# Kernel optimization log

Measured on AMD Instinct MI355X. Metric: run time of the kernel, lower is better.

Reference implementation:

```python
import jax, jax.numpy as jnp
import numpy as np

S, B, D = 2048, 2, 1024
NH, DH, DI = 16, 64, 4096


def setup_inputs() -> dict:
    key = jax.random.key(0)
    ks = jax.random.split(key, 12)
    init_qkv = 1.0 / np.sqrt(D)
    init_out = 1.0 / np.sqrt(NH * DH)
    stdm = 1.0 / np.sqrt(D)
    stdi = 1.0 / np.sqrt(DI)

    def u(k, shape, lo, hi):
        return jax.random.uniform(k, shape, jnp.float32, lo, hi)

    inp = {}
    inp["dec_inp"] = jax.random.normal(ks[0], (S, B, D), jnp.float32)
    # causal mask: True = masked (future key j > query i); shape [q, k, batch]
    causal = jnp.triu(jnp.ones((S, S), bool), k=1)
    inp["attn_mask"] = jnp.broadcast_to(causal[:, :, None], (S, S, B))
    inp["query_mean"] = u(ks[1], (NH * DH, D), -init_qkv, init_qkv)
    inp["key_mean"] = u(ks[2], (NH * DH, D), -init_qkv, init_qkv)
    inp["value_mean"] = u(ks[3], (NH * DH, D), -init_qkv, init_qkv)
    inp["query_std"] = u(ks[4], (NH * DH, D), 2 * np.log(init_qkv), np.log(init_qkv))
    inp["key_std"] = u(ks[5], (NH * DH, D), 2 * np.log(init_qkv), np.log(init_qkv))
    inp["value_std"] = u(ks[6], (NH * DH, D), 2 * np.log(init_qkv), np.log(init_qkv))
    inp["output_mean"] = u(ks[7], (D, NH * DH), -init_out, init_out)
    inp["output_std"] = u(ks[8], (D, NH * DH), 2 * np.log(init_out), np.log(init_out))
    inp["ln1_gamma"] = jnp.ones((D,), jnp.float32)
    inp["ln1_beta"] = jnp.zeros((D,), jnp.float32)
    inp["w1_mean"] = u(ks[9], (DI, D), -stdm, stdm)
    inp["w2_mean"] = u(ks[10], (D, DI), -stdi, stdi)
    inp["w1_std"] = u(ks[11], (DI, D), 2 * np.log(stdm), np.log(stdm))
    inp["w2_std"] = u(jax.random.fold_in(key, 99), (D, DI), 2 * np.log(stdi), np.log(stdi))
    inp["ln2_gamma"] = jnp.ones((D,), jnp.float32)
    inp["ln2_beta"] = jnp.zeros((D,), jnp.float32)
    return inp


def _layer_norm(x, g, b, eps=1e-5):
    mu = jnp.mean(x, -1, keepdims=True)
    var = jnp.mean((x - mu) ** 2, -1, keepdims=True)
    return g * (x - mu) * jax.lax.rsqrt(var + eps) + b


def _kl(theta_mean, theta_std):
    return jnp.mean(theta_mean ** 2 - 2.0 * theta_std + jnp.exp(2.0 * theta_std)) / 2.0


def reference(dec_inp, attn_mask, query_mean, key_mean, value_mean, query_std,
              key_std, value_std, output_mean, output_std, ln1_gamma, ln1_beta,
              w1_mean, w2_mean, w1_std, w2_std, ln2_gamma, ln2_beta):
    scale = 1.0 / (DH ** 0.5)
    # QKV projections (eval mode: no Bayesian weight sampling, diffs are 0)
    head_q = jnp.einsum('ibd,hd->ibh', dec_inp, query_mean).reshape(S, B, NH, DH)
    head_k = jnp.einsum('ibd,hd->ibh', dec_inp, key_mean).reshape(S, B, NH, DH)
    head_v = jnp.einsum('ibd,hd->ibh', dec_inp, value_mean).reshape(S, B, NH, DH)
    attn_score = jnp.einsum('ibnd,jbnd->ijbn', head_q, head_k) * scale
    attn_score = jnp.where(attn_mask[:, :, :, None], -jnp.inf, attn_score)
    attn_prob = jax.nn.softmax(attn_score, axis=1)  # softmax over key dim j
    attn_vec = jnp.einsum('ijbn,jbnd->ibnd', attn_prob, head_v).reshape(S, B, NH * DH)
    # NOTE: the original code (bug-faithfully) projects with value_mean, not output_mean
    attn_out = jnp.einsum('ibh,dh->ibd', attn_vec, value_mean)
    h = _layer_norm(dec_inp + attn_out, ln1_gamma, ln1_beta)
    attn_kl = _kl(
        jnp.concatenate([query_mean, key_mean, value_mean, output_mean.T], -1),
        jnp.concatenate([query_std, key_std, value_std, output_std.T], -1))
    # Bayesian positionwise FF (no activation in BayesPositionwiseFF)
    l1 = jnp.einsum('ibd,fd->ibf', h, w1_mean)
    l2 = jnp.einsum('ibf,df->ibd', l1, w2_mean)
    out = _layer_norm(h + l2, ln2_gamma, ln2_beta)
    ff_kl = _kl(jnp.concatenate([w1_mean, w2_mean.T], -1),
                jnp.concatenate([w1_std, w2_std.T], -1))
    return out, attn_kl + ff_kl
```

## Files before the change

### kernel.cpp

```cpp
#include <hip/hip_runtime.h>

#define S_LEN  2048
#define BATCH  2
#define DMODEL 1024
#define NHEADS 16
#define DHEAD  64
#define DFF    4096
#define MROWS  (S_LEN*BATCH)
#define QKVN   3072

typedef __attribute__((ext_vector_type(8))) short bf16x8;
typedef __attribute__((ext_vector_type(4))) float f32x4;
typedef __attribute__((ext_vector_type(4))) short s16x4;

#define NEG_BIG (-3.0e38f)
#define SCALE_LOG2 (0.125f * 1.4426950408889634f)

__device__ __forceinline__ short f2bf(float f){
  unsigned u = __float_as_uint(f);
  u += 0x7fffu + ((u >> 16) & 1u);
  return (short)(u >> 16);
}

__device__ __forceinline__ void gload16(const void* gptr, void* lptr){
  __builtin_amdgcn_global_load_lds(
      (const __attribute__((address_space(1))) unsigned int*)gptr,
      (__attribute__((address_space(3))) unsigned int*)lptr,
      16, 0, 0);
}

__global__ __launch_bounds__(256) void cast_kernel(const float* __restrict__ in,
                                                   short* __restrict__ out, int n){
  int i = (blockIdx.x * 256 + threadIdx.x) * 4;
  if (i >= n) return;
  f32x4 v = *(const f32x4*)(in + i);
  s16x4 o;
  o[0] = f2bf(v[0]); o[1] = f2bf(v[1]); o[2] = f2bf(v[2]); o[3] = f2bf(v[3]);
  *(s16x4*)(out + i) = o;
}

__global__ __launch_bounds__(256) void cast_kl_kernel(const float* __restrict__ mean,
                                                      const float* __restrict__ stdv,
                                                      short* __restrict__ outb,
                                                      int n, double* acc){
  __shared__ double red[4];
  double local = 0.0;
  const int stride = gridDim.x * 1024;
  for (int i = (blockIdx.x * 256 + threadIdx.x) * 4; i < n; i += stride){
    f32x4 m = *(const f32x4*)(mean + i);
    f32x4 sv = *(const f32x4*)(stdv + i);
    if (outb){
      s16x4 o;
      o[0] = f2bf(m[0]); o[1] = f2bf(m[1]); o[2] = f2bf(m[2]); o[3] = f2bf(m[3]);
      *(s16x4*)(outb + i) = o;
    }
    for (int e = 0; e < 4; e++)
      local += (double)(m[e] * m[e]) - 2.0 * (double)sv[e] + (double)expf(2.f * sv[e]);
  }
  for (int msk = 1; msk < 64; msk <<= 1) local += __shfl_xor(local, msk, 64);
  const int t = threadIdx.x;
  if ((t & 63) == 0) red[t >> 6] = local;
  __syncthreads();
  if (t == 0) atomicAdd(acc, red[0] + red[1] + red[2] + red[3]);
}

__global__ void kl_final(const double* acc, float* out){
  out[0] = (float)(acc[0] / 8388608.0 + acc[1] / 16777216.0);
}

template<int BN>
__global__ __launch_bounds__(512) void gemm_bt(const short* __restrict__ A,
                                               const short* __restrict__ Bt,
                                               float* __restrict__ Cf,
                                               short* __restrict__ Cb,
                                               int M, int N, int K, int nbx){
  __shared__ short As[4][128][32];
  __shared__ short Bs[4][BN][32];
  constexpr int NB = BN / 32;
  constexpr int BSTRIDE = BN * 64;
  const int t = threadIdx.x;
  const int lane = t & 63, w = t >> 6;
  const int q8 = (int)gridDim.x >> 3;
  const int sid = ((int)blockIdx.x & 7) * q8 + ((int)blockIdx.x >> 3);
  const int bx = sid % nbx, by = sid / nbx;
  const int m0 = by * 128, n0 = bx * BN;
  const int wm = (w & 3) * 32, wn = (w >> 2) * (BN / 2);
  const int lr = lane & 15, lg = lane >> 4;
  const bool doB = (BN == 128) || (t < 256);
  const bool twoLoads = (BN == 128) || (w < 4);

  f32x4 acc[2][NB] = {};

  const short* Ap = A  + (size_t)(m0 + (t >> 2)) * K + (t & 3) * 8;
  const short* Bp = Bt + (size_t)(n0 + ((t & (BN * 4 - 1)) >> 2)) * K + (t & 3) * 8;
  char* ldsA0 = (char*)As + w * 1024;
  char* ldsB0 = (char*)Bs + (w & (NB * 2 - 1)) * 1024;

  const int nk = K / 32;
  for (int p = 0; p < 3; p++){
    gload16(Ap + p * 32, ldsA0 + p * 8192);
    if (doB) gload16(Bp + p * 32, ldsB0 + p * BSTRIDE);
  }

  for (int kt = 0; kt < nk; kt++){
    const int rem = nk - 1 - kt;
    if (twoLoads){
      if (rem >= 2)      asm volatile("s_waitcnt vmcnt(4)" ::: "memory");
      else if (rem == 1) asm volatile("s_waitcnt vmcnt(2)" ::: "memory");
      else               asm volatile("s_waitcnt vmcnt(0)" ::: "memory");
    } else {
      if (rem >= 2)      asm volatile("s_waitcnt vmcnt(2)" ::: "memory");
      else if (rem == 1) asm volatile("s_waitcnt vmcnt(1)" ::: "memory");
      else               asm volatile("s_waitcnt vmcnt(0)" ::: "memory");
    }
    __builtin_amdgcn_s_barrier();
    asm volatile("" ::: "memory");

    const int nxt = kt + 3;
    if (nxt < nk){
      gload16(Ap + nxt * 32, ldsA0 + (nxt & 3) * 8192);
      if (doB) gload16(Bp + nxt * 32, ldsB0 + (nxt & 3) * BSTRIDE);
    }

    const int cur = kt & 3;
    bf16x8 a0 = *(const bf16x8*)&As[cur][wm      + lr][lg * 8];
    bf16x8 a1 = *(const bf16x8*)&As[cur][wm + 16 + lr][lg * 8];
    bf16x8 bfr[NB];
    for (int ni = 0; ni < NB; ni++)
      bfr[ni] = *(const bf16x8*)&Bs[cur][wn + ni * 16 + lr][lg * 8];
    __builtin_amdgcn_s_setprio(1);
    for (int ni = 0; ni < NB; ni++){
      acc[0][ni] = __builtin_amdgcn_mfma_f32_16x16x32_bf16(a0, bfr[ni], acc[0][ni], 0, 0, 0);
      acc[1][ni] = __builtin_amdgcn_mfma_f32_16x16x32_bf16(a1, bfr[ni], acc[1][ni], 0, 0, 0);
    }
    __builtin_amdgcn_s_setprio(0);
  }

  for (int mi = 0; mi < 2; mi++){
    for (int ni = 0; ni < NB; ni++){
      int row = m0 + wm + mi * 16 + lg * 4;
      int col = n0 + wn + ni * 16 + lr;
      for (int r = 0; r < 4; r++){
        float v = acc[mi][ni][r];
        if (Cf) Cf[(size_t)(row + r) * N + col] = v;
        if (Cb) Cb[(size_t)(row + r) * N + col] = f2bf(v);
      }
    }
  }
}

__global__ __launch_bounds__(256) void attn_kernel(const short* __restrict__ QKV,
                                                   short* __restrict__ AV){
  __shared__ short Ks[64][64];
  __shared__ short Vst[64][64];
  __shared__ short Pt[4][16][64];
  const int t = threadIdx.x, lane = t & 63, w = t >> 6;
  const int hb = blockIdx.y;
  const int b = hb >> 4, n = hb & 15;
  const int lr = lane & 15, lg = lane >> 4;

  const int qt = 31 - (int)blockIdx.x;
  const int q0w = qt * 64 + w * 16;

  bf16x8 aq[2];
  {
    const short* qp = QKV + ((size_t)(q0w + lr) * BATCH + b) * QKVN + n * DHEAD + lg * 8;
    aq[0] = *(const bf16x8*)(qp);
    aq[1] = *(const bf16x8*)(qp + 32);
  }

  f32x4 acc[4] = {};
  float m_run = NEG_BIG, l_run = 0.f;

  for (int jt = 0; jt <= qt; jt++){
    const int j0 = jt * 64;
    __syncthreads();
    {
      int j = t >> 2, u0 = (t & 3) * 2;
      const short* kp = QKV + ((size_t)(j0 + j) * BATCH + b) * QKVN + DMODEL + n * DHEAD + u0 * 8;
      *(bf16x8*)&Ks[j][(u0 ^ (j & 7)) * 8]       = *(const bf16x8*)(kp);
      *(bf16x8*)&Ks[j][((u0 + 1) ^ (j & 7)) * 8] = *(const bf16x8*)(kp + 8);
      int jv = t & 63, dq = (t >> 6) * 16;
      const short* vp = QKV + ((size_t)(j0 + jv) * BATCH + b) * QKVN + 2 * DMODEL + n * DHEAD + dq;
      bf16x8 v0 = *(const bf16x8*)(vp);
      bf16x8 v1 = *(const bf16x8*)(vp + 8);
      int uj = jv >> 3, jl = jv & 7;
      for (int e = 0; e < 8; e++){
        int sc = (((uj ^ e) << 3) | jl);
        Vst[dq + e][sc]     = v0[e];
        Vst[dq + 8 + e][sc] = v1[e];
      }
    }
    __syncthreads();

    f32x4 s[4];
    __builtin_amdgcn_s_setprio(1);
    for (int nf = 0; nf < 4; nf++){
      f32x4 z = {};
      for (int kk = 0; kk < 2; kk++){
        bf16x8 bk = *(const bf16x8*)&Ks[nf * 16 + lr][((kk * 4 + lg) ^ (lr & 7)) * 8];
        z = __builtin_amdgcn_mfma_f32_16x16x32_bf16(bk, aq[kk], z, 0, 0, 0);
      }
      s[nf] = z;
    }
    __builtin_amdgcn_s_setprio(0);

    if (jt == qt){
      int qg = q0w + lr;
      for (int nf = 0; nf < 4; nf++)
        for (int r = 0; r < 4; r++)
          if (j0 + nf * 16 + lg * 4 + r > qg) s[nf][r] = NEG_BIG;
    }

    float mx = NEG_BIG;
    for (int nf = 0; nf < 4; nf++){
      float a0 = fmaxf(s[nf][0], s[nf][1]);
      float a1 = fmaxf(s[nf][2], s[nf][3]);
      mx = fmaxf(mx, fmaxf(a0, a1));
    }
    mx = fmaxf(mx, __shfl_xor(mx, 16, 64));
    mx = fmaxf(mx, __shfl_xor(mx, 32, 64));
    float mxs = mx * SCALE_LOG2;

    if (__any(mxs > m_run + 8.f)){
      float mn = fmaxf(m_run, mxs);
      float corr = __builtin_exp2f(m_run - mn);
      m_run = mn;
      l_run *= corr;
      float cb[4];
      for (int r = 0; r < 4; r++) cb[r] = __shfl(corr, lg * 4 + r, 64);
      for (int df = 0; df < 4; df++)
        for (int r = 0; r < 4; r++) acc[df][r] *= cb[r];
    }

    float rs = 0.f;
    for (int nf = 0; nf < 4; nf++)
      for (int r = 0; r < 4; r++){
        float p = __builtin_exp2f(fmaf(s[nf][r], SCALE_LOG2, -m_run));
        s[nf][r] = p;
        rs += p;
      }
    rs += __shfl_xor(rs, 16, 64);
    rs += __shfl_xor(rs, 32, 64);
    l_run += rs;

    char* prow = (char*)&Pt[w][lr][0];
    for (int nf = 0; nf < 4; nf++){
      unsigned u0 = __float_as_uint(s[nf][0]);
      unsigned u1 = __float_as_uint(s[nf][1]);
      unsigned u2 = __float_as_uint(s[nf][2]);
      unsigned u3 = __float_as_uint(s[nf][3]);
      uint2 val;
      val.x = (u0 >> 16) | (u1 & 0xffff0000u);
      val.y = (u2 >> 16) | (u3 & 0xffff0000u);
      int off = ((((nf * 2) + (lg >> 1)) ^ (lr & 7)) << 4) + ((lg & 1) << 3);
      *(uint2*)(prow + off) = val;
    }

    __builtin_amdgcn_s_setprio(1);
    for (int kk = 0; kk < 2; kk++){
      bf16x8 pa = *(const bf16x8*)(prow + ((((kk * 4) + lg) ^ (lr & 7)) << 4));
      for (int df = 0; df < 4; df++){
        bf16x8 bv = *(const bf16x8*)&Vst[df * 16 + lr][((kk * 4 + lg) ^ (lr & 7)) * 8];
        acc[df] = __builtin_amdgcn_mfma_f32_16x16x32_bf16(pa, bv, acc[df], 0, 0, 0);
      }
    }
    __builtin_amdgcn_s_setprio(0);
  }

  float lb[4];
  for (int r = 0; r < 4; r++) lb[r] = __shfl(l_run, lg * 4 + r, 64);
  for (int df = 0; df < 4; df++){
    for (int r = 0; r < 4; r++){
      int i_glob = q0w + lg * 4 + r;
      AV[((size_t)i_glob * BATCH + b) * DMODEL + n * DHEAD + df * 16 + lr] =
          f2bf(acc[df][r] / lb[r]);
    }
  }
}

__global__ __launch_bounds__(256) void ln_kernel(const float* __restrict__ xa,
                                                 const float* __restrict__ xb,
                                                 const float* __restrict__ gamma,
                                                 const float* __restrict__ beta,
                                                 float* __restrict__ outF,
                                                 short* __restrict__ outB){
  __shared__ float red[4];
  const int row = blockIdx.x, t = threadIdx.x;
  const size_t base = (size_t)row * DMODEL + t * 4;
  f32x4 a  = *(const f32x4*)(xa + base);
  f32x4 bb = *(const f32x4*)(xb + base);
  f32x4 x;
  for (int e = 0; e < 4; e++) x[e] = a[e] + bb[e];
  float sum = x[0] + x[1] + x[2] + x[3];
  for (int m = 1; m < 64; m <<= 1) sum += __shfl_xor(sum, m, 64);
  if ((t & 63) == 0) red[t >> 6] = sum;
  __syncthreads();
  float mu = (red[0] + red[1] + red[2] + red[3]) * (1.f / DMODEL);
  float sq = 0.f;
  for (int e = 0; e < 4; e++){ float d = x[e] - mu; sq += d * d; }
  for (int m = 1; m < 64; m <<= 1) sq += __shfl_xor(sq, m, 64);
  __syncthreads();
  if ((t & 63) == 0) red[t >> 6] = sq;
  __syncthreads();
  float var = (red[0] + red[1] + red[2] + red[3]) * (1.f / DMODEL);
  float rstd = rsqrtf(var + 1e-5f);
  f32x4 g  = *(const f32x4*)(gamma + t * 4);
  f32x4 be = *(const f32x4*)(beta + t * 4);
  for (int e = 0; e < 4; e++){
    float y = g[e] * (x[e] - mu) * rstd + be[e];
    if (outF) outF[base + e] = y;
    if (outB) outB[base + e] = f2bf(y);
  }
}

extern "C" void kernel_launch(void* const* d_in, const int* in_sizes, int n_in,
                              void* d_out, int out_size, void* d_ws, size_t ws_size,
                              hipStream_t stream){
  (void)in_sizes; (void)n_in; (void)out_size; (void)ws_size;
  const float* dec = (const float*)d_in[0];
  const float* qm  = (const float*)d_in[2];
  const float* km  = (const float*)d_in[3];
  const float* vm  = (const float*)d_in[4];
  const float* qs  = (const float*)d_in[5];
  const float* ks  = (const float*)d_in[6];
  const float* vs  = (const float*)d_in[7];
  const float* om  = (const float*)d_in[8];
  const float* os_ = (const float*)d_in[9];
  const float* g1  = (const float*)d_in[10];
  const float* b1  = (const float*)d_in[11];
  const float* w1m = (const float*)d_in[12];
  const float* w2m = (const float*)d_in[13];
  const float* w1s = (const float*)d_in[14];
  const float* w2s = (const float*)d_in[15];
  const float* g2  = (const float*)d_in[16];
  const float* b2  = (const float*)d_in[17];
  float* out = (float*)d_out;

  char* ws = (char*)d_ws;
  size_t off = 0;
  auto alloc = [&](size_t bytes) -> char* {
    char* p = ws + off;
    off += (bytes + 255) & ~(size_t)255;
    return p;
  };
  short* Xb   = (short*)alloc((size_t)MROWS * DMODEL * 2);
  short* Wqkv = (short*)alloc((size_t)QKVN * DMODEL * 2);
  short* W1   = (short*)alloc((size_t)DFF * DMODEL * 2);
  short* W2   = (short*)alloc((size_t)DMODEL * DFF * 2);
  short* Wv   = Wqkv + (size_t)2 * DMODEL * DMODEL;
  short* QKVb = (short*)alloc((size_t)MROWS * QKVN * 2);
  short* AVb  = (short*)alloc((size_t)MROWS * DMODEL * 2);
  float* tmpF = (float*)alloc((size_t)MROWS * DMODEL * 4);
  float* hF   = (float*)alloc((size_t)MROWS * DMODEL * 4);
  double* acc = (double*)alloc(256);
  short* L1 = QKVb;

  hipMemsetAsync(acc, 0, 16, stream);

  cast_kernel<<<MROWS * DMODEL / 1024, 256, 0, stream>>>(dec, Xb, MROWS * DMODEL);
  cast_kl_kernel<<<1024, 256, 0, stream>>>(qm, qs, Wqkv, DMODEL * DMODEL, acc);
  cast_kl_kernel<<<1024, 256, 0, stream>>>(km, ks, Wqkv + (size_t)DMODEL * DMODEL, DMODEL * DMODEL, acc);
  cast_kl_kernel<<<1024, 256, 0, stream>>>(vm, vs, Wqkv + (size_t)2 * DMODEL * DMODEL, DMODEL * DMODEL, acc);
  cast_kl_kernel<<<1024, 256, 0, stream>>>(om, os_, nullptr, DMODEL * DMODEL, acc);
  cast_kl_kernel<<<1024, 256, 0, stream>>>(w1m, w1s, W1, DFF * DMODEL, acc + 1);
  cast_kl_kernel<<<1024, 256, 0, stream>>>(w2m, w2s, W2, DMODEL * DFF, acc + 1);

  gemm_bt<128><<<(QKVN / 128) * (MROWS / 128), 512, 0, stream>>>(Xb, Wqkv, nullptr, QKVb, MROWS, QKVN, DMODEL, QKVN / 128);

  attn_kernel<<<dim3(32, BATCH * NHEADS), 256, 0, stream>>>(QKVb, AVb);

  gemm_bt<64><<<(DMODEL / 64) * (MROWS / 128), 512, 0, stream>>>(AVb, Wv, tmpF, nullptr, MROWS, DMODEL, DMODEL, DMODEL / 64);

  ln_kernel<<<MROWS, 256, 0, stream>>>(dec, tmpF, g1, b1, hF, Xb);

  gemm_bt<128><<<(DFF / 128) * (MROWS / 128), 512, 0, stream>>>(Xb, W1, nullptr, L1, MROWS, DFF, DMODEL, DFF / 128);
  gemm_bt<64><<<(DMODEL / 64) * (MROWS / 128), 512, 0, stream>>>(L1, W2, tmpF, nullptr, MROWS, DMODEL, DFF, DMODEL / 64);

  ln_kernel<<<MROWS, 256, 0, stream>>>(hF, tmpF, g2, b2, out, nullptr);

  kl_final<<<1, 1, 0, stream>>>(acc, out + (size_t)MROWS * DMODEL);
}
```

Baseline: 565.9 us.

## Pair causal query tiles per attention block and use triple-buffered GEMM pipeline

The attention kernel now launches half as many blocks, and each block processes query tile i and tile 31-i so every block does the same amount of causal work, removing tail imbalance. Separately, the GEMM shared-memory pipeline drops from four stages to three, with a prefetch distance of two and simpler waitcnt logic. This reduces LDS use, which may allow more blocks per CU, but gives less load-latency hiding. The attention change also halves the grid to 512 blocks, which may leave the GPU less occupied.

```diff
diff --git a/kernel.cpp b/kernel.cpp
--- a/kernel.cpp
+++ b/kernel.cpp
@@ -74,8 +74,8 @@
                                                float* __restrict__ Cf,
                                                short* __restrict__ Cb,
                                                int M, int N, int K, int nbx){
-  __shared__ short As[4][128][32];
-  __shared__ short Bs[4][BN][32];
+  __shared__ short As[3][128][32];
+  __shared__ short Bs[3][BN][32];
   constexpr int NB = BN / 32;
   constexpr int BSTRIDE = BN * 64;
   const int t = threadIdx.x;
@@ -87,7 +87,6 @@
   const int wm = (w & 3) * 32, wn = (w >> 2) * (BN / 2);
   const int lr = lane & 15, lg = lane >> 4;
   const bool doB = (BN == 128) || (t < 256);
-  const bool twoLoads = (BN == 128) || (w < 4);
 
   f32x4 acc[2][NB] = {};
 
@@ -97,43 +96,40 @@
   char* ldsB0 = (char*)Bs + (w & (NB * 2 - 1)) * 1024;
 
   const int nk = K / 32;
-  for (int p = 0; p < 3; p++){
+  for (int p = 0; p < 2; p++){
     gload16(Ap + p * 32, ldsA0 + p * 8192);
     if (doB) gload16(Bp + p * 32, ldsB0 + p * BSTRIDE);
   }
 
+  int bufcur = 0;
   for (int kt = 0; kt < nk; kt++){
-    const int rem = nk - 1 - kt;
-    if (twoLoads){
-      if (rem >= 2)      asm volatile("s_waitcnt vmcnt(4)" ::: "memory");
-      else if (rem == 1) asm volatile("s_waitcnt vmcnt(2)" ::: "memory");
-      else               asm volatile("s_waitcnt vmcnt(0)" ::: "memory");
+    if (kt + 1 < nk){
+      if (doB) asm volatile("s_waitcnt vmcnt(2)" ::: "memory");
+      else     asm volatile("s_waitcnt vmcnt(1)" ::: "memory");
     } else {
-      if (rem >= 2)      asm volatile("s_waitcnt vmcnt(2)" ::: "memory");
-      else if (rem == 1) asm volatile("s_waitcnt vmcnt(1)" ::: "memory");
-      else               asm volatile("s_waitcnt vmcnt(0)" ::: "memory");
+      asm volatile("s_waitcnt vmcnt(0)" ::: "memory");
     }
     __builtin_amdgcn_s_barrier();
     asm volatile("" ::: "memory");
 
-    const int nxt = kt + 3;
-    if (nxt < nk){
-      gload16(Ap + nxt * 32, ldsA0 + (nxt & 3) * 8192);
-      if (doB) gload16(Bp + nxt * 32, ldsB0 + (nxt & 3) * BSTRIDE);
-    }
-
-    const int cur = kt & 3;
-    bf16x8 a0 = *(const bf16x8*)&As[cur][wm      + lr][lg * 8];
-    bf16x8 a1 = *(const bf16x8*)&As[cur][wm + 16 + lr][lg * 8];
+    if (kt + 2 < nk){
+      int bnx = bufcur >= 1 ? bufcur - 1 : bufcur + 2;
+      gload16(Ap + (kt + 2) * 32, ldsA0 + bnx * 8192);
+      if (doB) gload16(Bp + (kt + 2) * 32, ldsB0 + bnx * BSTRIDE);
+    }
+
+    bf16x8 a0 = *(const bf16x8*)&As[bufcur][wm      + lr][lg * 8];
+    bf16x8 a1 = *(const bf16x8*)&As[bufcur][wm + 16 + lr][lg * 8];
     bf16x8 bfr[NB];
     for (int ni = 0; ni < NB; ni++)
-      bfr[ni] = *(const bf16x8*)&Bs[cur][wn + ni * 16 + lr][lg * 8];
+      bfr[ni] = *(const bf16x8*)&Bs[bufcur][wn + ni * 16 + lr][lg * 8];
     __builtin_amdgcn_s_setprio(1);
     for (int ni = 0; ni < NB; ni++){
       acc[0][ni] = __builtin_amdgcn_mfma_f32_16x16x32_bf16(a0, bfr[ni], acc[0][ni], 0, 0, 0);
       acc[1][ni] = __builtin_amdgcn_mfma_f32_16x16x32_bf16(a1, bfr[ni], acc[1][ni], 0, 0, 0);
     }
     __builtin_amdgcn_s_setprio(0);
+    bufcur = bufcur < 2 ? bufcur + 1 : 0;
   }
 
   for (int mi = 0; mi < 2; mi++){
@@ -159,123 +155,126 @@
   const int b = hb >> 4, n = hb & 15;
   const int lr = lane & 15, lg = lane >> 4;
 
-  const int qt = 31 - (int)blockIdx.x;
-  const int q0w = qt * 64 + w * 16;
-
-  bf16x8 aq[2];
-  {
-    const short* qp = QKV + ((size_t)(q0w + lr) * BATCH + b) * QKVN + n * DHEAD + lg * 8;
-    aq[0] = *(const bf16x8*)(qp);
-    aq[1] = *(const bf16x8*)(qp + 32);
-  }
-
-  f32x4 acc[4] = {};
-  float m_run = NEG_BIG, l_run = 0.f;
-
-  for (int jt = 0; jt <= qt; jt++){
-    const int j0 = jt * 64;
+  for (int half = 0; half < 2; half++){
+    const int qt = half ? (31 - (int)blockIdx.x) : (int)blockIdx.x;
+    const int q0w = qt * 64 + w * 16;
+
+    bf16x8 aq[2];
+    {
+      const short* qp = QKV + ((size_t)(q0w + lr) * BATCH + b) * QKVN + n * DHEAD + lg * 8;
+      aq[0] = *(const bf16x8*)(qp);
+      aq[1] = *(const bf16x8*)(qp + 32);
+    }
+
+    f32x4 acc[4] = {};
+    float m_run = NEG_BIG, l_run = 0.f;
+
+    for (int jt = 0; jt <= qt; jt++){
+      const int j0 = jt * 64;
+      __syncthreads();
+      {
+        int j = t >> 2, u0 = (t & 3) * 2;
+        const short* kp = QKV + ((size_t)(j0 + j) * BATCH + b) * QKVN + DMODEL + n * DHEAD + u0 * 8;
+        *(bf16x8*)&Ks[j][(u0 ^ (j & 7)) * 8]       = *(const bf16x8*)(kp);
+        *(bf16x8*)&Ks[j][((u0 + 1) ^ (j & 7)) * 8] = *(const bf16x8*)(kp + 8);
+        int jv = t & 63, dq = (t >> 6) * 16;
+        const short* vp = QKV + ((size_t)(j0 + jv) * BATCH + b) * QKVN + 2 * DMODEL + n * DHEAD + dq;
+        bf16x8 v0 = *(const bf16x8*)(vp);
+        bf16x8 v1 = *(const bf16x8*)(vp + 8);
+        int uj = jv >> 3, jl = jv & 7;
+        for (int e = 0; e < 8; e++){
+          int sc = (((uj ^ e) << 3) | jl);
+          Vst[dq + e][sc]     = v0[e];
+          Vst[dq + 8 + e][sc] = v1[e];
+        }
+      }
+      __syncthreads();
+
+      f32x4 s[4];
+      __builtin_amdgcn_s_setprio(1);
+      for (int nf = 0; nf < 4; nf++){
+        f32x4 z = {};
+        for (int kk = 0; kk < 2; kk++){
+          bf16x8 bk = *(const bf16x8*)&Ks[nf * 16 + lr][((kk * 4 + lg) ^ (lr & 7)) * 8];
+          z = __builtin_amdgcn_mfma_f32_16x16x32_bf16(bk, aq[kk], z, 0, 0, 0);
+        }
+        s[nf] = z;
+      }
+      __builtin_amdgcn_s_setprio(0);
+
+      if (jt == qt){
+        int qg = q0w + lr;
+        for (int nf = 0; nf < 4; nf++)
+          for (int r = 0; r < 4; r++)
+            if (j0 + nf * 16 + lg * 4 + r > qg) s[nf][r] = NEG_BIG;
+      }
+
+      float mx = NEG_BIG;
+      for (int nf = 0; nf < 4; nf++){
+        float a0 = fmaxf(s[nf][0], s[nf][1]);
+        float a1 = fmaxf(s[nf][2], s[nf][3]);
+        mx = fmaxf(mx, fmaxf(a0, a1));
+      }
+      mx = fmaxf(mx, __shfl_xor(mx, 16, 64));
+      mx = fmaxf(mx, __shfl_xor(mx, 32, 64));
+      float mxs = mx * SCALE_LOG2;
+
+      if (__any(mxs > m_run + 8.f)){
+        float mn = fmaxf(m_run, mxs);
+        float corr = __builtin_exp2f(m_run - mn);
+        m_run = mn;
+        l_run *= corr;
+        float cb[4];
+        for (int r = 0; r < 4; r++) cb[r] = __shfl(corr, lg * 4 + r, 64);
+        for (int df = 0; df < 4; df++)
+          for (int r = 0; r < 4; r++) acc[df][r] *= cb[r];
+      }
+
+      float rs = 0.f;
+      for (int nf = 0; nf < 4; nf++)
+        for (int r = 0; r < 4; r++){
+          float p = __builtin_exp2f(fmaf(s[nf][r], SCALE_LOG2, -m_run));
+          s[nf][r] = p;
+          rs += p;
+        }
+      rs += __shfl_xor(rs, 16, 64);
+      rs += __shfl_xor(rs, 32, 64);
+      l_run += rs;
+
+      char* prow = (char*)&Pt[w][lr][0];
+      for (int nf = 0; nf < 4; nf++){
+        unsigned u0 = __float_as_uint(s[nf][0]);
+        unsigned u1 = __float_as_uint(s[nf][1]);
+        unsigned u2 = __float_as_uint(s[nf][2]);
+        unsigned u3 = __float_as_uint(s[nf][3]);
+        uint2 val;
+        val.x = (u0 >> 16) | (u1 & 0xffff0000u);
+        val.y = (u2 >> 16) | (u3 & 0xffff0000u);
+        int off = ((((nf * 2) + (lg >> 1)) ^ (lr & 7)) << 4) + ((lg & 1) << 3);
+        *(uint2*)(prow + off) = val;
+      }
+
+      __builtin_amdgcn_s_setprio(1);
+      for (int kk = 0; kk < 2; kk++){
+        bf16x8 pa = *(const bf16x8*)(prow + ((((kk * 4) + lg) ^ (lr & 7)) << 4));
+        for (int df = 0; df < 4; df++){
+          bf16x8 bv = *(const bf16x8*)&Vst[df * 16 + lr][((kk * 4 + lg) ^ (lr & 7)) * 8];
+          acc[df] = __builtin_amdgcn_mfma_f32_16x16x32_bf16(pa, bv, acc[df], 0, 0, 0);
+        }
+      }
+      __builtin_amdgcn_s_setprio(0);
+    }
+
+    float lb[4];
+    for (int r = 0; r < 4; r++) lb[r] = __shfl(l_run, lg * 4 + r, 64);
+    for (int df = 0; df < 4; df++){
+      for (int r = 0; r < 4; r++){
+        int i_glob = q0w + lg * 4 + r;
+        AV[((size_t)i_glob * BATCH + b) * DMODEL + n * DHEAD + df * 16 + lr] =
+            f2bf(acc[df][r] / lb[r]);
+      }
+    }
     __syncthreads();
-    {
-      int j = t >> 2, u0 = (t & 3) * 2;
-      const short* kp = QKV + ((size_t)(j0 + j) * BATCH + b) * QKVN + DMODEL + n * DHEAD + u0 * 8;
-      *(bf16x8*)&Ks[j][(u0 ^ (j & 7)) * 8]       = *(const bf16x8*)(kp);
-      *(bf16x8*)&Ks[j][((u0 + 1) ^ (j & 7)) * 8] = *(const bf16x8*)(kp + 8);
-      int jv = t & 63, dq = (t >> 6) * 16;
-      const short* vp = QKV + ((size_t)(j0 + jv) * BATCH + b) * QKVN + 2 * DMODEL + n * DHEAD + dq;
-      bf16x8 v0 = *(const bf16x8*)(vp);
-      bf16x8 v1 = *(const bf16x8*)(vp + 8);
-      int uj = jv >> 3, jl = jv & 7;
-      for (int e = 0; e < 8; e++){
-        int sc = (((uj ^ e) << 3) | jl);
-        Vst[dq + e][sc]     = v0[e];
-        Vst[dq + 8 + e][sc] = v1[e];
-      }
-    }
-    __syncthreads();
-
-    f32x4 s[4];
-    __builtin_amdgcn_s_setprio(1);
-    for (int nf = 0; nf < 4; nf++){
-      f32x4 z = {};
-      for (int kk = 0; kk < 2; kk++){
-        bf16x8 bk = *(const bf16x8*)&Ks[nf * 16 + lr][((kk * 4 + lg) ^ (lr & 7)) * 8];
-        z = __builtin_amdgcn_mfma_f32_16x16x32_bf16(bk, aq[kk], z, 0, 0, 0);
-      }
-      s[nf] = z;
-    }
-    __builtin_amdgcn_s_setprio(0);
-
-    if (jt == qt){
-      int qg = q0w + lr;
-      for (int nf = 0; nf < 4; nf++)
-        for (int r = 0; r < 4; r++)
-          if (j0 + nf * 16 + lg * 4 + r > qg) s[nf][r] = NEG_BIG;
-    }
-
-    float mx = NEG_BIG;
-    for (int nf = 0; nf < 4; nf++){
-      float a0 = fmaxf(s[nf][0], s[nf][1]);
-      float a1 = fmaxf(s[nf][2], s[nf][3]);
-      mx = fmaxf(mx, fmaxf(a0, a1));
-    }
-    mx = fmaxf(mx, __shfl_xor(mx, 16, 64));
-    mx = fmaxf(mx, __shfl_xor(mx, 32, 64));
-    float mxs = mx * SCALE_LOG2;
-
-    if (__any(mxs > m_run + 8.f)){
-      float mn = fmaxf(m_run, mxs);
-      float corr = __builtin_exp2f(m_run - mn);
-      m_run = mn;
-      l_run *= corr;
-      float cb[4];
-      for (int r = 0; r < 4; r++) cb[r] = __shfl(corr, lg * 4 + r, 64);
-      for (int df = 0; df < 4; df++)
-        for (int r = 0; r < 4; r++) acc[df][r] *= cb[r];
-    }
-
-    float rs = 0.f;
-    for (int nf = 0; nf < 4; nf++)
-      for (int r = 0; r < 4; r++){
-        float p = __builtin_exp2f(fmaf(s[nf][r], SCALE_LOG2, -m_run));
-        s[nf][r] = p;
-        rs += p;
-      }
-    rs += __shfl_xor(rs, 16, 64);
-    rs += __shfl_xor(rs, 32, 64);
-    l_run += rs;
-
-    char* prow = (char*)&Pt[w][lr][0];
-    for (int nf = 0; nf < 4; nf++){
-      unsigned u0 = __float_as_uint(s[nf][0]);
-      unsigned u1 = __float_as_uint(s[nf][1]);
-      unsigned u2 = __float_as_uint(s[nf][2]);
-      unsigned u3 = __float_as_uint(s[nf][3]);
-      uint2 val;
-      val.x = (u0 >> 16) | (u1 & 0xffff0000u);
-      val.y = (u2 >> 16) | (u3 & 0xffff0000u);
-      int off = ((((nf * 2) + (lg >> 1)) ^ (lr & 7)) << 4) + ((lg & 1) << 3);
-      *(uint2*)(prow + off) = val;
-    }
-
-    __builtin_amdgcn_s_setprio(1);
-    for (int kk = 0; kk < 2; kk++){
-      bf16x8 pa = *(const bf16x8*)(prow + ((((kk * 4) + lg) ^ (lr & 7)) << 4));
-      for (int df = 0; df < 4; df++){
-        bf16x8 bv = *(const bf16x8*)&Vst[df * 16 + lr][((kk * 4 + lg) ^ (lr & 7)) * 8];
-        acc[df] = __builtin_amdgcn_mfma_f32_16x16x32_bf16(pa, bv, acc[df], 0, 0, 0);
-      }
-    }
-    __builtin_amdgcn_s_setprio(0);
-  }
-
-  float lb[4];
-  for (int r = 0; r < 4; r++) lb[r] = __shfl(l_run, lg * 4 + r, 64);
-  for (int df = 0; df < 4; df++){
-    for (int r = 0; r < 4; r++){
-      int i_glob = q0w + lg * 4 + r;
-      AV[((size_t)i_glob * BATCH + b) * DMODEL + n * DHEAD + df * 16 + lr] =
-          f2bf(acc[df][r] / lb[r]);
-    }
   }
 }
 
@@ -368,7 +367,7 @@
 
   gemm_bt<128><<<(QKVN / 128) * (MROWS / 128), 512, 0, stream>>>(Xb, Wqkv, nullptr, QKVb, MROWS, QKVN, DMODEL, QKVN / 128);
 
-  attn_kernel<<<dim3(32, BATCH * NHEADS), 256, 0, stream>>>(QKVb, AVb);
+  attn_kernel<<<dim3(16, BATCH * NHEADS), 256, 0, stream>>>(QKVb, AVb);
 
   gemm_bt<64><<<(DMODEL / 64) * (MROWS / 128), 512, 0, stream>>>(AVb, Wv, tmpF, nullptr, MROWS, DMODEL, DMODEL, DMODEL / 64);
 
```

After: 535.3 us. -5.4%, faster.
